# Performance work log

Measured on AMD Instinct MI355X. Metric: run time of the kernel, lower is better.

The kernel has to match this reference:

```python
import jax, jax.numpy as jnp
import numpy as np

IN_DIM = 1024
D = 2048          # feedforward_dim
G = 8             # gate_count
OUT_DIM = 1024
N = 4096
GATE_SCALE = 0.9


def setup_inputs() -> dict:
    key = jax.random.key(0)
    k = jax.random.split(key, 7)
    x = jax.random.normal(k[0], (N, IN_DIM), dtype=jnp.float32)
    gate_ids = jax.random.randint(k[1], (N, 1), 0, G)
    W1 = jax.random.normal(k[2], (2 * (1 + G) * D, IN_DIM), dtype=jnp.float32) * 0.02
    b1 = jnp.zeros((2 * (1 + G) * D,), dtype=jnp.float32)
    W2 = jax.random.normal(k[3], (D, 2 * D), dtype=jnp.float32) * 0.02
    b2 = jnp.zeros((D,), dtype=jnp.float32)
    W3 = jax.random.normal(k[4], (OUT_DIM, D), dtype=jnp.float32) * 0.02
    return {"classification_input": x, "gate_ids": gate_ids,
            "W1": W1, "b1": b1, "W2": W2, "b2": b2, "W3": W3}


def reference(classification_input, gate_ids, W1, b1, W2, b2, W3):
    n = classification_input.shape[0]
    # l1 + relu: [N, (1+G)*2D]
    h = jax.nn.relu(classification_input @ W1.T + b1)
    # mask: gate blocks scaled by 0.9, shared block (last) always on
    onehot = jax.nn.one_hot(gate_ids[:, 0], G, dtype=h.dtype) * GATE_SCALE  # [N, G]
    mask = jnp.concatenate([onehot, jnp.ones((n, 1), dtype=h.dtype)], axis=1)  # [N, G+1]
    # masked block-sum over the (1+G) blocks of size 2D
    h = h.reshape(n, 1 + G, 2 * D)
    s = jnp.einsum('ngd,ng->nd', h, mask)  # [N, 2D]
    h2 = jax.nn.relu(s @ W2.T + b2)        # [N, D]
    return h2 @ W3.T                        # [N, OUT_DIM]
```

## Files before the change

kernel.cpp:

```cpp
#include <hip/hip_runtime.h>
#include <cstdint>


#define NP 5120
#define NROWT 40
#define NROWS 4096
#define GATES 8

typedef short short8 __attribute__((ext_vector_type(8)));
typedef unsigned short ushort8v __attribute__((ext_vector_type(8)));
typedef float f32x4 __attribute__((ext_vector_type(4)));

constexpr int BM = 128, BN = 128, BK = 32;
constexpr int LDSW_FB = 40;

__device__ __forceinline__ unsigned short f2b(float f) {
    __bf16 h = (__bf16)f;
    return __builtin_bit_cast(unsigned short, h);
}

__device__ __forceinline__ void gload_lds16(const void* g, void* l) {
    __builtin_amdgcn_global_load_lds(
        (const __attribute__((address_space(1))) void*)g,
        (__attribute__((address_space(3))) void*)l, 16, 0, 0);
}


__global__ void bucket_kernel(const int* __restrict__ gid,
                              int* __restrict__ perm,
                              int* __restrict__ tile_gate,
                              unsigned short* __restrict__ zrow)
{
    __shared__ int cnt[GATES], pstart[GATES], cur[GATES];
    const int t = threadIdx.x;
    if (zrow) {
        ushort4 z; z.x = 0; z.y = 0; z.z = 0; z.w = 0;
        ((ushort4*)zrow)[t] = z;
    }
    if (t < GATES) cnt[t] = 0;
    __syncthreads();
    for (int i = t; i < NROWS; i += 256) atomicAdd(&cnt[gid[i]], 1);
    __syncthreads();
    if (t == 0) {
        int off = 0;
        for (int g = 0; g < GATES; g++) {
            pstart[g] = off;
            cur[g] = 0;
            off += (cnt[g] + 127) & ~127;
        }
    }
    __syncthreads();
    for (int i = t; i < NP; i += 256) perm[i] = -1;
    if (t < NROWT) {
        int r0 = t * 128;
        int tg = 0;
        for (int g = 0; g < GATES; g++) {
            int pc = (cnt[g] + 127) & ~127;
            if (r0 >= pstart[g] && r0 < pstart[g] + pc) tg = g;
        }
        tile_gate[t] = tg;
    }
    __syncthreads();
    for (int i = t; i < NROWS; i += 256) {
        int g = gid[i];
        int p = atomicAdd(&cur[g], 1);
        perm[pstart[g] + p] = i;
    }
}

__global__ __launch_bounds__(256)
void cast_kernel(const float* __restrict__ src, unsigned short* __restrict__ dst,
                 int n8)
{
    int i = blockIdx.x * 256 + threadIdx.x;
    const int stride = gridDim.x * 256;
    for (; i < n8; i += stride) {
        const float4* s4 = (const float4*)(src + (size_t)i * 8);
        float4 a = s4[0], b = s4[1];
        ushort8v v;
        v[0] = f2b(a.x); v[1] = f2b(a.y); v[2] = f2b(a.z); v[3] = f2b(a.w);
        v[4] = f2b(b.x); v[5] = f2b(b.y); v[6] = f2b(b.z); v[7] = f2b(b.w);
        *(ushort8v*)(dst + (size_t)i * 8) = v;
    }
}

__global__ __launch_bounds__(256, 2)
void l1_fast(const unsigned short* __restrict__ xbf,
             const unsigned short* __restrict__ W1bf,
             const float* __restrict__ b1,
             const int* __restrict__ perm,
             const int* __restrict__ tile_gate,
             unsigned short* __restrict__ s_out)
{
    __shared__ __align__(16) unsigned short As[BM][BK];
    __shared__ __align__(16) unsigned short Bg[BN][BK];
    __shared__ __align__(16) unsigned short Bs[BN][BK];

    const int t = threadIdx.x;
    const int rbase = blockIdx.y * BM;
    const int cbase = blockIdx.x * BN;
    const int gate = tile_gate[blockIdx.y];

    const int srow  = t >> 2;
    const int skcol = ((t & 3) ^ ((t >> 3) & 3)) * 8;

    int g0 = perm[rbase + srow];      if (g0 < 0) g0 = NROWS;
    int g1 = perm[rbase + srow + 64]; if (g1 < 0) g1 = NROWS;

    const unsigned short* a0 = xbf + (size_t)g0 * 1024 + skcol;
    const unsigned short* a1 = xbf + (size_t)g1 * 1024 + skcol;
    const unsigned short* bg0 = W1bf + ((size_t)(gate * 4096 + cbase + srow)) * 1024 + skcol;
    const unsigned short* bg1 = bg0 + (size_t)64 * 1024;
    const unsigned short* bs0 = W1bf + ((size_t)(GATES * 4096 + cbase + srow)) * 1024 + skcol;
    const unsigned short* bs1 = bs0 + (size_t)64 * 1024;

    const int wchunk = (t >> 6) * 1024;

    f32x4 accg[4][4], accs[4][4];
#pragma unroll
    for (int m = 0; m < 4; m++)
#pragma unroll
        for (int n = 0; n < 4; n++) {
            accg[m][n] = (f32x4){0.f, 0.f, 0.f, 0.f};
            accs[m][n] = (f32x4){0.f, 0.f, 0.f, 0.f};
        }

    const int lane = t & 63;
    const int wid  = t >> 6;
    const int wr = wid >> 1, wc = wid & 1;
    const int lr = lane & 15;
    const int kb = (((lane >> 4) ^ ((lr >> 1) & 3))) * 8;

    for (int k0 = 0; k0 < 1024; k0 += BK) {
        gload_lds16(a0 + k0,  (char*)As + wchunk);
        gload_lds16(a1 + k0,  (char*)As + wchunk + 4096);
        gload_lds16(bg0 + k0, (char*)Bg + wchunk);
        gload_lds16(bg1 + k0, (char*)Bg + wchunk + 4096);
        gload_lds16(bs0 + k0, (char*)Bs + wchunk);
        gload_lds16(bs1 + k0, (char*)Bs + wchunk + 4096);
        __syncthreads();

        short8 af[4];
#pragma unroll
        for (int m = 0; m < 4; m++)
            af[m] = *(const short8*)&As[wr * 64 + m * 16 + lr][kb];
        {
            short8 bf[4];
#pragma unroll
            for (int n = 0; n < 4; n++)
                bf[n] = *(const short8*)&Bg[wc * 64 + n * 16 + lr][kb];
#pragma unroll
            for (int m = 0; m < 4; m++)
#pragma unroll
                for (int n = 0; n < 4; n++)
                    accg[m][n] = __builtin_amdgcn_mfma_f32_16x16x32_bf16(
                        af[m], bf[n], accg[m][n], 0, 0, 0);
        }
        {
            short8 bf[4];
#pragma unroll
            for (int n = 0; n < 4; n++)
                bf[n] = *(const short8*)&Bs[wc * 64 + n * 16 + lr][kb];
#pragma unroll
            for (int m = 0; m < 4; m++)
#pragma unroll
                for (int n = 0; n < 4; n++)
                    accs[m][n] = __builtin_amdgcn_mfma_f32_16x16x32_bf16(
                        af[m], bf[n], accs[m][n], 0, 0, 0);
        }
        __syncthreads();
    }

    const int rowoff = (lane >> 4) * 4;
#pragma unroll
    for (int m = 0; m < 4; m++) {
        const int prow = rbase + wr * 64 + m * 16 + rowoff;
#pragma unroll
        for (int n = 0; n < 4; n++) {
            const int col = cbase + wc * 64 + n * 16 + lr;
            const float b1g = b1[(size_t)gate * 4096 + col];
            const float b1s = b1[(size_t)GATES * 4096 + col];
#pragma unroll
            for (int j = 0; j < 4; j++) {
                float vg = accg[m][n][j] + b1g;
                float vs = accs[m][n][j] + b1s;
                float sv = 0.9f * fmaxf(vg, 0.f) + fmaxf(vs, 0.f);
                s_out[(size_t)(prow + j) * 4096 + col] = f2b(sv);
            }
        }
    }
}

__global__ __launch_bounds__(256, 2)
void l2_fast(const unsigned short* __restrict__ s_in,
             const unsigned short* __restrict__ W2bf,
             const float* __restrict__ b2,
             unsigned short* __restrict__ h2)
{
    __shared__ __align__(16) unsigned short As[BM][BK];
    __shared__ __align__(16) unsigned short Bt[BN][BK];

    const int t = threadIdx.x;
    const int rbase = blockIdx.y * BM;
    const int cbase = blockIdx.x * BN;
    const int srow  = t >> 2;
    const int skcol = ((t & 3) ^ ((t >> 3) & 3)) * 8;

    const unsigned short* a0 = s_in + (size_t)(rbase + srow) * 4096 + skcol;
    const unsigned short* a1 = a0 + (size_t)64 * 4096;
    const unsigned short* b0 = W2bf + (size_t)(cbase + srow) * 4096 + skcol;
    const unsigned short* b1p = b0 + (size_t)64 * 4096;

    const int wchunk = (t >> 6) * 1024;

    f32x4 acc[4][4];
#pragma unroll
    for (int m = 0; m < 4; m++)
#pragma unroll
        for (int n = 0; n < 4; n++) acc[m][n] = (f32x4){0.f, 0.f, 0.f, 0.f};

    const int lane = t & 63;
    const int wid  = t >> 6;
    const int wr = wid >> 1, wc = wid & 1;
    const int lr = lane & 15;
    const int kb = (((lane >> 4) ^ ((lr >> 1) & 3))) * 8;

    for (int k0 = 0; k0 < 4096; k0 += BK) {
        gload_lds16(a0 + k0,  (char*)As + wchunk);
        gload_lds16(a1 + k0,  (char*)As + wchunk + 4096);
        gload_lds16(b0 + k0,  (char*)Bt + wchunk);
        gload_lds16(b1p + k0, (char*)Bt + wchunk + 4096);
        __syncthreads();

        short8 af[4], bf[4];
#pragma unroll
        for (int m = 0; m < 4; m++)
            af[m] = *(const short8*)&As[wr * 64 + m * 16 + lr][kb];
#pragma unroll
        for (int n = 0; n < 4; n++)
            bf[n] = *(const short8*)&Bt[wc * 64 + n * 16 + lr][kb];
#pragma unroll
        for (int m = 0; m < 4; m++)
#pragma unroll
            for (int n = 0; n < 4; n++)
                acc[m][n] = __builtin_amdgcn_mfma_f32_16x16x32_bf16(
                    af[m], bf[n], acc[m][n], 0, 0, 0);
        __syncthreads();
    }

    const int rowoff = (lane >> 4) * 4;
#pragma unroll
    for (int m = 0; m < 4; m++) {
        const int prow = rbase + wr * 64 + m * 16 + rowoff;
#pragma unroll
        for (int n = 0; n < 4; n++) {
            const int col = cbase + wc * 64 + n * 16 + lr;
            const float bb = b2[col];
#pragma unroll
            for (int j = 0; j < 4; j++) {
                float v = fmaxf(acc[m][n][j] + bb, 0.f);
                h2[(size_t)(prow + j) * 2048 + col] = f2b(v);
            }
        }
    }
}

__global__ __launch_bounds__(256, 2)
void l3_fast(const unsigned short* __restrict__ h2,
             const unsigned short* __restrict__ W3bf,
             const int* __restrict__ perm,
             float* __restrict__ out)
{
    __shared__ __align__(16) unsigned short As[BM][BK];
    __shared__ __align__(16) unsigned short Bt[BN][BK];

    const int t = threadIdx.x;
    const int rbase = blockIdx.y * BM;
    const int cbase = blockIdx.x * BN;
    const int srow  = t >> 2;
    const int skcol = ((t & 3) ^ ((t >> 3) & 3)) * 8;

    const unsigned short* a0 = h2 + (size_t)(rbase + srow) * 2048 + skcol;
    const unsigned short* a1 = a0 + (size_t)64 * 2048;
    const unsigned short* b0 = W3bf + (size_t)(cbase + srow) * 2048 + skcol;
    const unsigned short* b1p = b0 + (size_t)64 * 2048;

    const int wchunk = (t >> 6) * 1024;

    f32x4 acc[4][4];
#pragma unroll
    for (int m = 0; m < 4; m++)
#pragma unroll
        for (int n = 0; n < 4; n++) acc[m][n] = (f32x4){0.f, 0.f, 0.f, 0.f};

    const int lane = t & 63;
    const int wid  = t >> 6;
    const int wr = wid >> 1, wc = wid & 1;
    const int lr = lane & 15;
    const int kb = (((lane >> 4) ^ ((lr >> 1) & 3))) * 8;

    for (int k0 = 0; k0 < 2048; k0 += BK) {
        gload_lds16(a0 + k0,  (char*)As + wchunk);
        gload_lds16(a1 + k0,  (char*)As + wchunk + 4096);
        gload_lds16(b0 + k0,  (char*)Bt + wchunk);
        gload_lds16(b1p + k0, (char*)Bt + wchunk + 4096);
        __syncthreads();

        short8 af[4], bf[4];
#pragma unroll
        for (int m = 0; m < 4; m++)
            af[m] = *(const short8*)&As[wr * 64 + m * 16 + lr][kb];
#pragma unroll
        for (int n = 0; n < 4; n++)
            bf[n] = *(const short8*)&Bt[wc * 64 + n * 16 + lr][kb];
#pragma unroll
        for (int m = 0; m < 4; m++)
#pragma unroll
            for (int n = 0; n < 4; n++)
                acc[m][n] = __builtin_amdgcn_mfma_f32_16x16x32_bf16(
                    af[m], bf[n], acc[m][n], 0, 0, 0);
        __syncthreads();
    }

    const int rowoff = (lane >> 4) * 4;
#pragma unroll
    for (int m = 0; m < 4; m++) {
        const int prow = rbase + wr * 64 + m * 16 + rowoff;
#pragma unroll
        for (int n = 0; n < 4; n++) {
            const int col = cbase + wc * 64 + n * 16 + lr;
#pragma unroll
            for (int j = 0; j < 4; j++) {
                int orow = perm[prow + j];
                if (orow >= 0)
                    out[(size_t)orow * 1024 + col] = acc[m][n][j];
            }
        }
    }
}

__global__ __launch_bounds__(256, 2)
void l1_fb(const float* __restrict__ x, const float* __restrict__ W1,
           const float* __restrict__ b1, const int* __restrict__ perm,
           const int* __restrict__ tile_gate, unsigned short* __restrict__ s_out)
{
    __shared__ __align__(16) unsigned short As[BM][LDSW_FB];
    __shared__ __align__(16) unsigned short Bg[BN][LDSW_FB];
    __shared__ __align__(16) unsigned short Bs[BN][LDSW_FB];

    const int t = threadIdx.x;
    const int rbase = blockIdx.y * BM;
    const int cbase = blockIdx.x * BN;
    const int gate = tile_gate[blockIdx.y];
    const int srow_t = t >> 3;
    const int scol   = (t & 7) * 4;

    int grow[4];
#pragma unroll
    for (int rr = 0; rr < 4; rr++) grow[rr] = perm[rbase + rr * 32 + srow_t];

    const float* Bgp = W1 + ((size_t)gate * 4096 + cbase) * 1024;
    const float* Bsp = W1 + ((size_t)GATES * 4096 + cbase) * 1024;

    f32x4 accg[4][4], accs[4][4];
#pragma unroll
    for (int m = 0; m < 4; m++)
#pragma unroll
        for (int n = 0; n < 4; n++) {
            accg[m][n] = (f32x4){0.f, 0.f, 0.f, 0.f};
            accs[m][n] = (f32x4){0.f, 0.f, 0.f, 0.f};
        }

    const int lane = t & 63;
    const int wid  = t >> 6;
    const int wr = wid >> 1, wc = wid & 1;
    const int lr = lane & 15;
    const int kb = (lane >> 4) * 8;

    for (int k0 = 0; k0 < 1024; k0 += BK) {
        __syncthreads();
#pragma unroll
        for (int rr = 0; rr < 4; rr++) {
            const int row = rr * 32 + srow_t;
            float4 av = make_float4(0.f, 0.f, 0.f, 0.f);
            if (grow[rr] >= 0)
                av = *(const float4*)(x + (size_t)grow[rr] * 1024 + k0 + scol);
            ushort4 pa;
            pa.x = f2b(av.x); pa.y = f2b(av.y); pa.z = f2b(av.z); pa.w = f2b(av.w);
            *(ushort4*)&As[row][scol] = pa;

            float4 gv = *(const float4*)(Bgp + (size_t)row * 1024 + k0 + scol);
            ushort4 pg;
            pg.x = f2b(gv.x); pg.y = f2b(gv.y); pg.z = f2b(gv.z); pg.w = f2b(gv.w);
            *(ushort4*)&Bg[row][scol] = pg;

            float4 sv = *(const float4*)(Bsp + (size_t)row * 1024 + k0 + scol);
            ushort4 ps;
            ps.x = f2b(sv.x); ps.y = f2b(sv.y); ps.z = f2b(sv.z); ps.w = f2b(sv.w);
            *(ushort4*)&Bs[row][scol] = ps;
        }
        __syncthreads();

        short8 af[4], bgf[4], bsf[4];
#pragma unroll
        for (int m = 0; m < 4; m++)
            af[m] = *(const short8*)&As[wr * 64 + m * 16 + lr][kb];
#pragma unroll
        for (int n = 0; n < 4; n++) {
            bgf[n] = *(const short8*)&Bg[wc * 64 + n * 16 + lr][kb];
            bsf[n] = *(const short8*)&Bs[wc * 64 + n * 16 + lr][kb];
        }
#pragma unroll
        for (int m = 0; m < 4; m++)
#pragma unroll
            for (int n = 0; n < 4; n++) {
                accg[m][n] = __builtin_amdgcn_mfma_f32_16x16x32_bf16(
                    af[m], bgf[n], accg[m][n], 0, 0, 0);
                accs[m][n] = __builtin_amdgcn_mfma_f32_16x16x32_bf16(
                    af[m], bsf[n], accs[m][n], 0, 0, 0);
            }
    }

    const int rowoff = (lane >> 4) * 4;
#pragma unroll
    for (int m = 0; m < 4; m++) {
        const int prow = rbase + wr * 64 + m * 16 + rowoff;
#pragma unroll
        for (int n = 0; n < 4; n++) {
            const int col = cbase + wc * 64 + n * 16 + lr;
            const float b1g = b1[(size_t)gate * 4096 + col];
            const float b1s = b1[(size_t)GATES * 4096 + col];
#pragma unroll
            for (int j = 0; j < 4; j++) {
                float vg = accg[m][n][j] + b1g;
                float vs = accs[m][n][j] + b1s;
                float sv = 0.9f * fmaxf(vg, 0.f) + fmaxf(vs, 0.f);
                s_out[(size_t)(prow + j) * 4096 + col] = f2b(sv);
            }
        }
    }
}

__global__ __launch_bounds__(256, 2)
void l2_fb(const unsigned short* __restrict__ s_in, const float* __restrict__ W2,
           const float* __restrict__ b2, unsigned short* __restrict__ h2)
{
    __shared__ __align__(16) unsigned short As[BM][LDSW_FB];
    __shared__ __align__(16) unsigned short Bt[BN][LDSW_FB];

    const int t = threadIdx.x;
    const int rbase = blockIdx.y * BM;
    const int cbase = blockIdx.x * BN;
    const int srow_t = t >> 3;
    const int scol   = (t & 7) * 4;

    f32x4 acc[4][4];
#pragma unroll
    for (int m = 0; m < 4; m++)
#pragma unroll
        for (int n = 0; n < 4; n++) acc[m][n] = (f32x4){0.f, 0.f, 0.f, 0.f};

    const int lane = t & 63;
    const int wid  = t >> 6;
    const int wr = wid >> 1, wc = wid & 1;
    const int lr = lane & 15;
    const int kb = (lane >> 4) * 8;

    for (int k0 = 0; k0 < 4096; k0 += BK) {
        __syncthreads();
#pragma unroll
        for (int rr = 0; rr < 4; rr++) {
            const int row = rr * 32 + srow_t;
            ushort4 av = *(const ushort4*)(s_in + (size_t)(rbase + row) * 4096 + k0 + scol);
            *(ushort4*)&As[row][scol] = av;
            float4 bv = *(const float4*)(W2 + (size_t)(cbase + row) * 4096 + k0 + scol);
            ushort4 pb;
            pb.x = f2b(bv.x); pb.y = f2b(bv.y); pb.z = f2b(bv.z); pb.w = f2b(bv.w);
            *(ushort4*)&Bt[row][scol] = pb;
        }
        __syncthreads();

        short8 af[4], bf[4];
#pragma unroll
        for (int m = 0; m < 4; m++)
            af[m] = *(const short8*)&As[wr * 64 + m * 16 + lr][kb];
#pragma unroll
        for (int n = 0; n < 4; n++)
            bf[n] = *(const short8*)&Bt[wc * 64 + n * 16 + lr][kb];
#pragma unroll
        for (int m = 0; m < 4; m++)
#pragma unroll
            for (int n = 0; n < 4; n++)
                acc[m][n] = __builtin_amdgcn_mfma_f32_16x16x32_bf16(
                    af[m], bf[n], acc[m][n], 0, 0, 0);
    }

    const int rowoff = (lane >> 4) * 4;
#pragma unroll
    for (int m = 0; m < 4; m++) {
        const int prow = rbase + wr * 64 + m * 16 + rowoff;
#pragma unroll
        for (int n = 0; n < 4; n++) {
            const int col = cbase + wc * 64 + n * 16 + lr;
            const float bb = b2[col];
#pragma unroll
            for (int j = 0; j < 4; j++) {
                float v = fmaxf(acc[m][n][j] + bb, 0.f);
                h2[(size_t)(prow + j) * 2048 + col] = f2b(v);
            }
        }
    }
}

__global__ __launch_bounds__(256, 2)
void l3_fb(const unsigned short* __restrict__ h2, const float* __restrict__ W3,
           const int* __restrict__ perm, float* __restrict__ out)
{
    __shared__ __align__(16) unsigned short As[BM][LDSW_FB];
    __shared__ __align__(16) unsigned short Bt[BN][LDSW_FB];

    const int t = threadIdx.x;
    const int rbase = blockIdx.y * BM;
    const int cbase = blockIdx.x * BN;
    const int srow_t = t >> 3;
    const int scol   = (t & 7) * 4;

    f32x4 acc[4][4];
#pragma unroll
    for (int m = 0; m < 4; m++)
#pragma unroll
        for (int n = 0; n < 4; n++) acc[m][n] = (f32x4){0.f, 0.f, 0.f, 0.f};

    const int lane = t & 63;
    const int wid  = t >> 6;
    const int wr = wid >> 1, wc = wid & 1;
    const int lr = lane & 15;
    const int kb = (lane >> 4) * 8;

    for (int k0 = 0; k0 < 2048; k0 += BK) {
        __syncthreads();
#pragma unroll
        for (int rr = 0; rr < 4; rr++) {
            const int row = rr * 32 + srow_t;
            ushort4 av = *(const ushort4*)(h2 + (size_t)(rbase + row) * 2048 + k0 + scol);
            *(ushort4*)&As[row][scol] = av;
            float4 bv = *(const float4*)(W3 + (size_t)(cbase + row) * 2048 + k0 + scol);
            ushort4 pb;
            pb.x = f2b(bv.x); pb.y = f2b(bv.y); pb.z = f2b(bv.z); pb.w = f2b(bv.w);
            *(ushort4*)&Bt[row][scol] = pb;
        }
        __syncthreads();

        short8 af[4], bf[4];
#pragma unroll
        for (int m = 0; m < 4; m++)
            af[m] = *(const short8*)&As[wr * 64 + m * 16 + lr][kb];
#pragma unroll
        for (int n = 0; n < 4; n++)
            bf[n] = *(const short8*)&Bt[wc * 64 + n * 16 + lr][kb];
#pragma unroll
        for (int m = 0; m < 4; m++)
#pragma unroll
            for (int n = 0; n < 4; n++)
                acc[m][n] = __builtin_amdgcn_mfma_f32_16x16x32_bf16(
                    af[m], bf[n], acc[m][n], 0, 0, 0);
    }

    const int rowoff = (lane >> 4) * 4;
#pragma unroll
    for (int m = 0; m < 4; m++) {
        const int prow = rbase + wr * 64 + m * 16 + rowoff;
#pragma unroll
        for (int n = 0; n < 4; n++) {
            const int col = cbase + wc * 64 + n * 16 + lr;
#pragma unroll
            for (int j = 0; j < 4; j++) {
                int orow = perm[prow + j];
                if (orow >= 0)
                    out[(size_t)orow * 1024 + col] = acc[m][n][j];
            }
        }
    }
}

extern "C" void kernel_launch(void* const* d_in, const int* in_sizes, int n_in,
                              void* d_out, int out_size, void* d_ws, size_t ws_size,
                              hipStream_t stream)
{
    const float* x   = (const float*)d_in[0];
    const int*   gid = (const int*)d_in[1];
    const float* W1  = (const float*)d_in[2];
    const float* b1  = (const float*)d_in[3];
    const float* W2  = (const float*)d_in[4];
    const float* b2  = (const float*)d_in[5];
    const float* W3  = (const float*)d_in[6];
    float* out = (float*)d_out;
    char* ws = (char*)d_ws;

    auto alignup = [](size_t v) { return (v + 255) & ~(size_t)255; };

    size_t off = 0;
    const size_t perm_off = off; off = alignup(off + (size_t)NP * 4);
    const size_t tg_off   = off; off = alignup(off + (size_t)NROWT * 4);
    const size_t xbf_off  = off; off = alignup(off + (size_t)4097 * 1024 * 2);
    const size_t w1_off   = off; off = alignup(off + (size_t)36864 * 1024 * 2);
    const size_t w2_off   = off; off = alignup(off + (size_t)2048 * 4096 * 2);
    const size_t w3_off   = off; off = alignup(off + (size_t)1024 * 2048 * 2);
    const size_t sB_off   = off; off = alignup(off + (size_t)NP * 4096 * 2);
    const size_t h2B_off  = off; off = alignup(off + (size_t)NP * 2048 * 2);
    const size_t need_big = off;

    const size_t sS_off   = 32768;
    const size_t h2S_off  = sS_off + (size_t)NP * 4096 * 2;
    const size_t need_sm  = h2S_off + (size_t)NP * 2048 * 2;

    int* perm = (int*)(ws + perm_off);
    int* tile_gate = (int*)(ws + tg_off);

    if (ws_size >= need_big) {
        unsigned short* xbf  = (unsigned short*)(ws + xbf_off);
        unsigned short* w1bf = (unsigned short*)(ws + w1_off);
        unsigned short* w2bf = (unsigned short*)(ws + w2_off);
        unsigned short* w3bf = (unsigned short*)(ws + w3_off);
        unsigned short* s_perm = (unsigned short*)(ws + sB_off);
        unsigned short* h2 = (unsigned short*)(ws + h2B_off);
        unsigned short* zrow = xbf + (size_t)NROWS * 1024;

        bucket_kernel<<<1, 256, 0, stream>>>(gid, perm, tile_gate, zrow);
        cast_kernel<<<2048, 256, 0, stream>>>(x,  xbf,  (NROWS * 1024) / 8);
        cast_kernel<<<2048, 256, 0, stream>>>(W1, w1bf, (36864 * 1024) / 8);
        cast_kernel<<<2048, 256, 0, stream>>>(W2, w2bf, (2048 * 4096) / 8);
        cast_kernel<<<1024, 256, 0, stream>>>(W3, w3bf, (1024 * 2048) / 8);
        l1_fast<<<dim3(32, NROWT), 256, 0, stream>>>(xbf, w1bf, b1, perm, tile_gate, s_perm);
        l2_fast<<<dim3(16, NROWT), 256, 0, stream>>>(s_perm, w2bf, b2, h2);
        l3_fast<<<dim3(8, NROWT), 256, 0, stream>>>(h2, w3bf, perm, out);
    } else if (ws_size >= need_sm) {
        unsigned short* s_perm = (unsigned short*)(ws + sS_off);
        unsigned short* h2 = (unsigned short*)(ws + h2S_off);

        bucket_kernel<<<1, 256, 0, stream>>>(gid, perm, tile_gate, (unsigned short*)nullptr);
        l1_fb<<<dim3(32, NROWT), 256, 0, stream>>>(x, W1, b1, perm, tile_gate, s_perm);
        l2_fb<<<dim3(16, NROWT), 256, 0, stream>>>(s_perm, W2, b2, h2);
        l3_fb<<<dim3(8, NROWT), 256, 0, stream>>>(h2, W3, perm, out);
    }
}
```

Measured before the change: 542.5 us.

## Fuse weight casts, remap blocks across XCDs, skip padding tiles, narrow l3 tiles

Merges the four fp32-to-bf16 cast launches into one kernel. Adds an XCD-aware block index remap to the three GEMM kernels for better L2 locality. Lets tiles made up entirely of padding rows exit early. Halves the l3 column tile to 64 with higher occupancy so more blocks fill the GPU. Costs are extra index arithmetic, one perm read per block, and lower per-block reuse in l3.

```diff
diff --git a/kernel.cpp b/kernel.cpp
--- a/kernel.cpp
+++ b/kernel.cpp
@@ -12,6 +12,7 @@
 typedef float f32x4 __attribute__((ext_vector_type(4)));
 
 constexpr int BM = 128, BN = 128, BK = 32;
+constexpr int BN3 = 64;
 constexpr int LDSW_FB = 40;
 
 __device__ __forceinline__ unsigned short f2b(float f) {
@@ -23,6 +24,14 @@
     __builtin_amdgcn_global_load_lds(
         (const __attribute__((address_space(1))) void*)g,
         (__attribute__((address_space(3))) void*)l, 16, 0, 0);
+}
+
+__device__ __forceinline__ void xcd_remap(int gx, int& bx, int& by) {
+    const int n = gx * gridDim.y;
+    const int lin = by * gx + bx;
+    const int s = (lin & 7) * (n >> 3) + (lin >> 3);
+    bx = s % gx;
+    by = s / gx;
 }
 
 
@@ -69,18 +78,27 @@
 }
 
 __global__ __launch_bounds__(256)
-void cast_kernel(const float* __restrict__ src, unsigned short* __restrict__ dst,
-                 int n8)
-{
+void cast_all_kernel(const float* __restrict__ s0, unsigned short* __restrict__ d0, int n0,
+                     const float* __restrict__ s1, unsigned short* __restrict__ d1, int n1,
+                     const float* __restrict__ s2, unsigned short* __restrict__ d2, int n2,
+                     const float* __restrict__ s3, unsigned short* __restrict__ d3, int n3)
+{
+    const int e01 = n0 + n1, e012 = n0 + n1 + n2;
+    const int total = e012 + n3;
     int i = blockIdx.x * 256 + threadIdx.x;
     const int stride = gridDim.x * 256;
-    for (; i < n8; i += stride) {
-        const float4* s4 = (const float4*)(src + (size_t)i * 8);
+    for (; i < total; i += stride) {
+        const float* s; unsigned short* d; int j;
+        if (i < n0)        { s = s0; d = d0; j = i; }
+        else if (i < e01)  { s = s1; d = d1; j = i - n0; }
+        else if (i < e012) { s = s2; d = d2; j = i - e01; }
+        else               { s = s3; d = d3; j = i - e012; }
+        const float4* s4 = (const float4*)(s + (size_t)j * 8);
         float4 a = s4[0], b = s4[1];
         ushort8v v;
         v[0] = f2b(a.x); v[1] = f2b(a.y); v[2] = f2b(a.z); v[3] = f2b(a.w);
         v[4] = f2b(b.x); v[5] = f2b(b.y); v[6] = f2b(b.z); v[7] = f2b(b.w);
-        *(ushort8v*)(dst + (size_t)i * 8) = v;
+        *(ushort8v*)(d + (size_t)j * 8) = v;
     }
 }
 
@@ -96,11 +114,14 @@
     __shared__ __align__(16) unsigned short Bg[BN][BK];
     __shared__ __align__(16) unsigned short Bs[BN][BK];
 
+    int bx = blockIdx.x, by = blockIdx.y;
+    xcd_remap(32, bx, by);
+    const int rbase = by * BM;
+    if (perm[rbase] < 0) return;
+    const int cbase = bx * BN;
+    const int gate = tile_gate[by];
+
     const int t = threadIdx.x;
-    const int rbase = blockIdx.y * BM;
-    const int cbase = blockIdx.x * BN;
-    const int gate = tile_gate[blockIdx.y];
-
     const int srow  = t >> 2;
     const int skcol = ((t & 3) ^ ((t >> 3) & 3)) * 8;
 
@@ -195,14 +216,19 @@
 void l2_fast(const unsigned short* __restrict__ s_in,
              const unsigned short* __restrict__ W2bf,
              const float* __restrict__ b2,
+             const int* __restrict__ perm,
              unsigned short* __restrict__ h2)
 {
     __shared__ __align__(16) unsigned short As[BM][BK];
     __shared__ __align__(16) unsigned short Bt[BN][BK];
 
+    int bx = blockIdx.x, by = blockIdx.y;
+    xcd_remap(16, bx, by);
+    const int rbase = by * BM;
+    if (perm[rbase] < 0) return;
+    const int cbase = bx * BN;
+
     const int t = threadIdx.x;
-    const int rbase = blockIdx.y * BM;
-    const int cbase = blockIdx.x * BN;
     const int srow  = t >> 2;
     const int skcol = ((t & 3) ^ ((t >> 3) & 3)) * 8;
 
@@ -265,33 +291,36 @@
     }
 }
 
-__global__ __launch_bounds__(256, 2)
+__global__ __launch_bounds__(256, 4)
 void l3_fast(const unsigned short* __restrict__ h2,
              const unsigned short* __restrict__ W3bf,
              const int* __restrict__ perm,
              float* __restrict__ out)
 {
     __shared__ __align__(16) unsigned short As[BM][BK];
-    __shared__ __align__(16) unsigned short Bt[BN][BK];
+    __shared__ __align__(16) unsigned short Bt[BN3][BK];
+
+    int bx = blockIdx.x, by = blockIdx.y;
+    xcd_remap(16, bx, by);
+    const int rbase = by * BM;
+    if (perm[rbase] < 0) return;
+    const int cbase = bx * BN3;
 
     const int t = threadIdx.x;
-    const int rbase = blockIdx.y * BM;
-    const int cbase = blockIdx.x * BN;
     const int srow  = t >> 2;
     const int skcol = ((t & 3) ^ ((t >> 3) & 3)) * 8;
 
     const unsigned short* a0 = h2 + (size_t)(rbase + srow) * 2048 + skcol;
     const unsigned short* a1 = a0 + (size_t)64 * 2048;
     const unsigned short* b0 = W3bf + (size_t)(cbase + srow) * 2048 + skcol;
-    const unsigned short* b1p = b0 + (size_t)64 * 2048;
 
     const int wchunk = (t >> 6) * 1024;
 
-    f32x4 acc[4][4];
+    f32x4 acc[4][2];
 #pragma unroll
     for (int m = 0; m < 4; m++)
 #pragma unroll
-        for (int n = 0; n < 4; n++) acc[m][n] = (f32x4){0.f, 0.f, 0.f, 0.f};
+        for (int n = 0; n < 2; n++) acc[m][n] = (f32x4){0.f, 0.f, 0.f, 0.f};
 
     const int lane = t & 63;
     const int wid  = t >> 6;
@@ -300,23 +329,22 @@
     const int kb = (((lane >> 4) ^ ((lr >> 1) & 3))) * 8;
 
     for (int k0 = 0; k0 < 2048; k0 += BK) {
-        gload_lds16(a0 + k0,  (char*)As + wchunk);
-        gload_lds16(a1 + k0,  (char*)As + wchunk + 4096);
-        gload_lds16(b0 + k0,  (char*)Bt + wchunk);
-        gload_lds16(b1p + k0, (char*)Bt + wchunk + 4096);
-        __syncthreads();
-
-        short8 af[4], bf[4];
+        gload_lds16(a0 + k0, (char*)As + wchunk);
+        gload_lds16(a1 + k0, (char*)As + wchunk + 4096);
+        gload_lds16(b0 + k0, (char*)Bt + wchunk);
+        __syncthreads();
+
+        short8 af[4], bf[2];
 #pragma unroll
         for (int m = 0; m < 4; m++)
             af[m] = *(const short8*)&As[wr * 64 + m * 16 + lr][kb];
 #pragma unroll
-        for (int n = 0; n < 4; n++)
-            bf[n] = *(const short8*)&Bt[wc * 64 + n * 16 + lr][kb];
-#pragma unroll
-        for (int m = 0; m < 4; m++)
-#pragma unroll
-            for (int n = 0; n < 4; n++)
+        for (int n = 0; n < 2; n++)
+            bf[n] = *(const short8*)&Bt[wc * 32 + n * 16 + lr][kb];
+#pragma unroll
+        for (int m = 0; m < 4; m++)
+#pragma unroll
+            for (int n = 0; n < 2; n++)
                 acc[m][n] = __builtin_amdgcn_mfma_f32_16x16x32_bf16(
                     af[m], bf[n], acc[m][n], 0, 0, 0);
         __syncthreads();
@@ -327,8 +355,8 @@
     for (int m = 0; m < 4; m++) {
         const int prow = rbase + wr * 64 + m * 16 + rowoff;
 #pragma unroll
-        for (int n = 0; n < 4; n++) {
-            const int col = cbase + wc * 64 + n * 16 + lr;
+        for (int n = 0; n < 2; n++) {
+            const int col = cbase + wc * 32 + n * 16 + lr;
 #pragma unroll
             for (int j = 0; j < 4; j++) {
                 int orow = perm[prow + j];
@@ -627,13 +655,14 @@
         unsigned short* zrow = xbf + (size_t)NROWS * 1024;
 
         bucket_kernel<<<1, 256, 0, stream>>>(gid, perm, tile_gate, zrow);
-        cast_kernel<<<2048, 256, 0, stream>>>(x,  xbf,  (NROWS * 1024) / 8);
-        cast_kernel<<<2048, 256, 0, stream>>>(W1, w1bf, (36864 * 1024) / 8);
-        cast_kernel<<<2048, 256, 0, stream>>>(W2, w2bf, (2048 * 4096) / 8);
-        cast_kernel<<<1024, 256, 0, stream>>>(W3, w3bf, (1024 * 2048) / 8);
+        cast_all_kernel<<<2048, 256, 0, stream>>>(
+            x,  xbf,  (NROWS * 1024) / 8,
+            W1, w1bf, (36864 * 1024) / 8,
+            W2, w2bf, (2048 * 4096) / 8,
+            W3, w3bf, (1024 * 2048) / 8);
         l1_fast<<<dim3(32, NROWT), 256, 0, stream>>>(xbf, w1bf, b1, perm, tile_gate, s_perm);
-        l2_fast<<<dim3(16, NROWT), 256, 0, stream>>>(s_perm, w2bf, b2, h2);
-        l3_fast<<<dim3(8, NROWT), 256, 0, stream>>>(h2, w3bf, perm, out);
+        l2_fast<<<dim3(16, NROWT), 256, 0, stream>>>(s_perm, w2bf, b2, perm, h2);
+        l3_fast<<<dim3(16, NROWT), 256, 0, stream>>>(h2, w3bf, perm, out);
     } else if (ws_size >= need_sm) {
         unsigned short* s_perm = (unsigned short*)(ws + sS_off);
         unsigned short* h2 = (unsigned short*)(ws + h2S_off);
```

Measured after the change: 549.0 us. Within noise of the previous version (+1.2%).
